# Kernel tuning notes

Measured on AMD Instinct MI355X. Metric: run time of the kernel, lower is better.

The kernel has to match this reference:

```python
import jax, jax.numpy as jnp
import numpy as np

N_NODES = 40000
N_EDGES = 640000
N_GRAPHS = 64
D_IN = 128
D_H = 128
N_LAYERS = 3
EPS = 1e-5


def _layer_norm(x, g, b):
    mu = jnp.mean(x, axis=-1, keepdims=True)
    var = jnp.var(x, axis=-1, keepdims=True)
    return (x - mu) * jax.lax.rsqrt(var + EPS) * g + b


def _sage_conv(x, src, dst, Wl, bl, Wr):
    # mean aggregation of neighbor messages: i <- mean_{j: (j->i)} x_j
    msg = x[src]                                              # [E, d]
    agg = jax.ops.segment_sum(msg, dst, num_segments=N_NODES)  # [N, d]
    deg = jax.ops.segment_sum(jnp.ones((src.shape[0],), x.dtype), dst,
                              num_segments=N_NODES)
    agg = agg / jnp.clip(deg, 1.0)[:, None]
    # out = lin_l(agg) + lin_r(x)
    return agg @ Wl.T + bl + x @ Wr.T


def setup_inputs() -> dict:
    key = jax.random.key(0)
    ks = jax.random.split(key, 12)
    s = 0.05
    x = jax.random.normal(ks[0], (N_NODES, D_IN), jnp.float32)
    edge_index = jax.random.randint(ks[1], (2, N_EDGES), 0, N_NODES, jnp.int64)
    batch = jnp.sort(jax.random.randint(ks[2], (N_NODES,), 0, N_GRAPHS, jnp.int64))
    fc_w = jax.random.normal(ks[3], (D_H, D_IN), jnp.float32) * s
    fc_b = jax.random.normal(ks[4], (D_H,), jnp.float32) * s
    Wl = jax.random.normal(ks[5], (N_LAYERS, D_H, D_H), jnp.float32) * s
    bl = jax.random.normal(ks[6], (N_LAYERS, D_H), jnp.float32) * s
    Wr = jax.random.normal(ks[7], (N_LAYERS, D_H, D_H), jnp.float32) * s
    ln_g = jnp.ones((N_LAYERS - 1, D_H), jnp.float32)
    ln_b = jnp.zeros((N_LAYERS - 1, D_H), jnp.float32)
    return {"x": x, "edge_index": edge_index, "batch": batch,
            "fc_w": fc_w, "fc_b": fc_b, "Wl": Wl, "bl": bl, "Wr": Wr,
            "ln_g": ln_g, "ln_b": ln_b}


def reference(x, edge_index, batch, fc_w, fc_b, Wl, bl, Wr, ln_g, ln_b):
    src, dst = edge_index[0], edge_index[1]
    # input projection + ReLU
    h = jax.nn.relu(x @ fc_w.T + fc_b)
    # GraphSAGE stack: norm + ReLU between layers, none after the last
    for i in range(N_LAYERS):
        h = _sage_conv(h, src, dst, Wl[i], bl[i], Wr[i])
        if i < N_LAYERS - 1:
            h = jax.nn.relu(_layer_norm(h, ln_g[i], ln_b[i]))
    node_embed = h                                            # [N, D_H]
    graph_embed = jax.ops.segment_sum(node_embed, batch,
                                      num_segments=N_GRAPHS)  # [G, D_H]
    return node_embed, graph_embed
```

## Files before the change

kernel.cpp:

```cpp
#include <hip/hip_runtime.h>
#include <hip/hip_bf16.h>


#define N_NODES 40000
#define N_EDGES 640000
#define N_GRAPHS 64
#define D 128
#define NODE_ELEMS 5120000
#define N_TILES 1250
#define ELL_W 64

typedef __hip_bfloat16 bf16;
typedef __attribute__((ext_vector_type(8))) short bf16x8;
typedef __attribute__((ext_vector_type(4))) float f32x4;

__device__ __forceinline__ float b2f(bf16 v) { return __bfloat162float(v); }
__device__ __forceinline__ bf16 f2b(float v) { return __float2bfloat16(v); }
__device__ __forceinline__ float lo2f(unsigned w) { return __uint_as_float(w << 16); }
__device__ __forceinline__ float hi2f(unsigned w) { return __uint_as_float(w & 0xffff0000u); }
__device__ __forceinline__ unsigned packbf(float a, float b) {
    union { bf16 h[2]; unsigned u; } c;
    c.h[0] = f2b(a); c.h[1] = f2b(b);
    return c.u;
}
__device__ __forceinline__ unsigned char f2e4m3(float v) {
    unsigned u = __float_as_uint(v * 0x1p-120f);
    unsigned r = (u + 0x0007ffffu + ((u >> 20) & 1u)) >> 20;
    return (unsigned char)min(r, 0x7eu);
}
__device__ __forceinline__ int is_bf16(const unsigned* lng) {
    return (lng[0] == 0x3f803f80u) ? 1 : 0;
}
__device__ __forceinline__ int edge_is_i64(const void* edge) {
    const unsigned* ew = (const unsigned*)edge;
    return (ew[1] == 0u && ew[3] == 0u && ew[5] == 0u) ? 1 : 0;
}

union U8 { uint4 u; bf16x8 s; };

template <int ISB>
__device__ __forceinline__ bf16x8 load8t(const void* base, long idx) {
    if (ISB) {
        U8 t;
        t.u = *(const uint4*)((const bf16*)base + idx);
        return t.s;
    }
    const float* f = (const float*)base + idx;
    float4 f0 = *(const float4*)f;
    float4 f1 = *(const float4*)(f + 4);
    union { bf16 h[8]; bf16x8 s; } t;
    t.h[0] = f2b(f0.x); t.h[1] = f2b(f0.y); t.h[2] = f2b(f0.z); t.h[3] = f2b(f0.w);
    t.h[4] = f2b(f1.x); t.h[5] = f2b(f1.y); t.h[6] = f2b(f1.z); t.h[7] = f2b(f1.w);
    return t.s;
}

template <int ISB>
__device__ __forceinline__ void proj_body(
    const void* __restrict__ X, const void* __restrict__ fcw,
    const void* __restrict__ fcb, bf16* __restrict__ outb,
    unsigned char* __restrict__ out8, int id, int t,
    bf16 (*sb)[128], unsigned char (*s8)[128]) {
    const int lane = t & 63;
    const int wave = t >> 6;
    const int n = lane & 15, q = lane >> 4;
    const int rowgrp = wave >> 1;
    const int cb = (wave & 1) * 64;
    const f32x4 zero = {0.f, 0.f, 0.f, 0.f};

    bf16x8 wf[4][4];
#pragma unroll
    for (int ct = 0; ct < 4; ct++)
#pragma unroll
        for (int ks = 0; ks < 4; ks++)
            wf[ct][ks] = load8t<ISB>(fcw, (long)(cb + ct * 16 + n) * 128 + ks * 32 + q * 8);
    float bz[4];
#pragma unroll
    for (int ct = 0; ct < 4; ct++)
        bz[ct] = ISB ? b2f(((const bf16*)fcb)[cb + ct * 16 + n])
                     : ((const float*)fcb)[cb + ct * 16 + n];

    for (int tile = id; tile < N_TILES; tile += 512) {
        const long rbase = (long)tile * 32 + rowgrp * 16 + n;
        f32x4 acc[4] = {zero, zero, zero, zero};
        bf16x8 af[4];
#pragma unroll
        for (int ks = 0; ks < 4; ks++)
            af[ks] = load8t<ISB>(X, rbase * 128 + ks * 32 + q * 8);
#pragma unroll
        for (int ct = 0; ct < 4; ct++)
#pragma unroll
            for (int ks = 0; ks < 4; ks++)
                acc[ct] = __builtin_amdgcn_mfma_f32_16x16x32_bf16(
                    af[ks], wf[ct][ks], acc[ct], 0, 0, 0);
#pragma unroll
        for (int ct = 0; ct < 4; ct++) {
            const int col = cb + ct * 16 + n;
#pragma unroll
            for (int r = 0; r < 4; r++) {
                const int rl = rowgrp * 16 + q * 4 + r;
                float v = fmaxf(acc[ct][r] + bz[ct], 0.f);
                sb[rl][col] = f2b(v);
                s8[rl][col] = f2e4m3(v);
            }
        }
        __syncthreads();
        {
            uint4* ob = (uint4*)((char*)outb + (size_t)tile * 8192);
            ob[t] = ((const uint4*)sb)[t];
            ob[t + 256] = ((const uint4*)sb)[t + 256];
            ((uint4*)(out8 + (size_t)tile * 4096))[t] = ((const uint4*)s8)[t];
        }
        __syncthreads();
    }
}

#define CW2_TOTAL 99200
__global__ __launch_bounds__(256, 2) void k_main(
    const void* __restrict__ X, const void* __restrict__ fcw,
    const void* __restrict__ fcb, bf16* __restrict__ outb,
    unsigned char* __restrict__ out8,
    const void* __restrict__ edge, const void* __restrict__ batch,
    const void* Wl, const void* bl, const void* Wr,
    const void* lng, const void* lnb,
    int* __restrict__ cursor, unsigned short* __restrict__ ell,
    int* __restrict__ batch32, bf16* __restrict__ cw,
    float* __restrict__ gsum) {
    __shared__ bf16 sb[32][128];
    __shared__ unsigned char s8[32][128];
    const int bid = blockIdx.x, t = threadIdx.x;
    int role, id;
    if (bid < 1000) { role = (bid & 1) ? 0 : 1; id = bid >> 1; }
    else if (bid < 1012) { role = 0; id = 500 + (bid - 1000); }
    else if (bid < 1169) { role = 2; id = bid - 1012; }
    else { role = 3; id = bid - 1169; }

    if (role == 1) {
        const int i64 = edge_is_i64(edge);
        int s[5], d[5];
#pragma unroll
        for (int i = 0; i < 5; i++) {
            int e = id * 1280 + i * 256 + t;
            if (i64) {
                s[i] = (int)((const long long*)edge)[e];
                d[i] = (int)((const long long*)edge)[N_EDGES + e];
            } else {
                s[i] = ((const int*)edge)[e];
                d[i] = ((const int*)edge)[N_EDGES + e];
            }
        }
        int p[5];
#pragma unroll
        for (int i = 0; i < 5; i++) p[i] = atomicAdd(&cursor[d[i]], 1);
#pragma unroll
        for (int i = 0; i < 5; i++)
            if (p[i] < ELL_W) ell[d[i] * ELL_W + p[i]] = (unsigned short)s[i];
        return;
    }
    if (role == 2) {
        int j = id * 256 + t;
        if (j < N_NODES)
            batch32[j] = edge_is_i64(edge) ? (int)((const long long*)batch)[j]
                                           : ((const int*)batch)[j];
        return;
    }
    if (role == 3) {
        int i = id * 256 + t;
        if (i >= CW2_TOTAL) return;
        int isb = is_bf16((const unsigned*)lng);
        const void* s; int o;
        if (i < 49152)       { s = Wl;  o = i; }
        else if (i < 49536)  { s = bl;  o = i - 49152; }
        else if (i < 98688)  { s = Wr;  o = i - 49536; }
        else if (i < 98944)  { s = lng; o = i - 98688; }
        else                 { s = lnb; o = i - 98944; }
        cw[i] = isb ? ((const bf16*)s)[o] : f2b(((const float*)s)[o]);
        return;
    }

    {
        int i = id * 256 + t;
        if (i < N_GRAPHS * D) gsum[i] = 0.f;
    }
    if (is_bf16((const unsigned*)lng))
        proj_body<1>(X, fcw, fcb, outb, out8, id, t, sb, s8);
    else
        proj_body<0>(X, fcw, fcb, outb, out8, id, t, sb, s8);
}

__global__ __launch_bounds__(256, 6) void k_agg8(
    const unsigned char* __restrict__ h8, const int* __restrict__ cursor,
    const unsigned short* __restrict__ ell, bf16* __restrict__ agg) {
    const int qw = threadIdx.x >> 4;
    const int l16 = threadIdx.x & 15;
    const int nodeA = blockIdx.x * 32 + qw * 2;
    const int nodeB = nodeA + 1;
    const int degA = min(cursor[nodeA], ELL_W);
    const int degB = min(cursor[nodeB], ELL_W);
    const int dmax = max(degA, degB);
    const uint4* rA = (const uint4*)(ell + (size_t)nodeA * ELL_W);
    const uint4* rB = (const uint4*)(ell + (size_t)nodeB * ELL_W);
    const uint2* hp = (const uint2*)h8;
    float aA[8] = {0.f, 0.f, 0.f, 0.f, 0.f, 0.f, 0.f, 0.f};
    float aB[8] = {0.f, 0.f, 0.f, 0.f, 0.f, 0.f, 0.f, 0.f};
    for (int e = 0; e < dmax; e += 8) {
        const uint4 ia = rA[e >> 3];
        const uint4 ib = rB[e >> 3];
        uint2 gA[8], gB[8];
        gA[0] = hp[(size_t)(ia.x & 0xffffu) * 16 + l16];
        gA[1] = hp[(size_t)(ia.x >> 16) * 16 + l16];
        gA[2] = hp[(size_t)(ia.y & 0xffffu) * 16 + l16];
        gA[3] = hp[(size_t)(ia.y >> 16) * 16 + l16];
        gA[4] = hp[(size_t)(ia.z & 0xffffu) * 16 + l16];
        gA[5] = hp[(size_t)(ia.z >> 16) * 16 + l16];
        gA[6] = hp[(size_t)(ia.w & 0xffffu) * 16 + l16];
        gA[7] = hp[(size_t)(ia.w >> 16) * 16 + l16];
        gB[0] = hp[(size_t)(ib.x & 0xffffu) * 16 + l16];
        gB[1] = hp[(size_t)(ib.x >> 16) * 16 + l16];
        gB[2] = hp[(size_t)(ib.y & 0xffffu) * 16 + l16];
        gB[3] = hp[(size_t)(ib.y >> 16) * 16 + l16];
        gB[4] = hp[(size_t)(ib.z & 0xffffu) * 16 + l16];
        gB[5] = hp[(size_t)(ib.z >> 16) * 16 + l16];
        gB[6] = hp[(size_t)(ib.w & 0xffffu) * 16 + l16];
        gB[7] = hp[(size_t)(ib.w >> 16) * 16 + l16];
#pragma unroll
        for (int i = 0; i < 8; i++) {
            const float mA = (e + i < degA) ? 0x1p120f : 0.f;
            aA[0] = fmaf(mA, __uint_as_float((gA[i].x << 20) & 0x07f00000u), aA[0]);
            aA[1] = fmaf(mA, __uint_as_float((gA[i].x << 12) & 0x07f00000u), aA[1]);
            aA[2] = fmaf(mA, __uint_as_float((gA[i].x << 4)  & 0x07f00000u), aA[2]);
            aA[3] = fmaf(mA, __uint_as_float((gA[i].x >> 4)  & 0x07f00000u), aA[3]);
            aA[4] = fmaf(mA, __uint_as_float((gA[i].y << 20) & 0x07f00000u), aA[4]);
            aA[5] = fmaf(mA, __uint_as_float((gA[i].y << 12) & 0x07f00000u), aA[5]);
            aA[6] = fmaf(mA, __uint_as_float((gA[i].y << 4)  & 0x07f00000u), aA[6]);
            aA[7] = fmaf(mA, __uint_as_float((gA[i].y >> 4)  & 0x07f00000u), aA[7]);
        }
#pragma unroll
        for (int i = 0; i < 8; i++) {
            const float mB = (e + i < degB) ? 0x1p120f : 0.f;
            aB[0] = fmaf(mB, __uint_as_float((gB[i].x << 20) & 0x07f00000u), aB[0]);
            aB[1] = fmaf(mB, __uint_as_float((gB[i].x << 12) & 0x07f00000u), aB[1]);
            aB[2] = fmaf(mB, __uint_as_float((gB[i].x << 4)  & 0x07f00000u), aB[2]);
            aB[3] = fmaf(mB, __uint_as_float((gB[i].x >> 4)  & 0x07f00000u), aB[3]);
            aB[4] = fmaf(mB, __uint_as_float((gB[i].y << 20) & 0x07f00000u), aB[4]);
            aB[5] = fmaf(mB, __uint_as_float((gB[i].y << 12) & 0x07f00000u), aB[5]);
            aB[6] = fmaf(mB, __uint_as_float((gB[i].y << 4)  & 0x07f00000u), aB[6]);
            aB[7] = fmaf(mB, __uint_as_float((gB[i].y >> 4)  & 0x07f00000u), aB[7]);
        }
    }
    const float invA = 1.f / (float)max(degA, 1);
    const float invB = 1.f / (float)max(degB, 1);
    uint4 oA, oB;
    oA.x = packbf(aA[0] * invA, aA[1] * invA);
    oA.y = packbf(aA[2] * invA, aA[3] * invA);
    oA.z = packbf(aA[4] * invA, aA[5] * invA);
    oA.w = packbf(aA[6] * invA, aA[7] * invA);
    oB.x = packbf(aB[0] * invB, aB[1] * invB);
    oB.y = packbf(aB[2] * invB, aB[3] * invB);
    oB.z = packbf(aB[4] * invB, aB[5] * invB);
    oB.w = packbf(aB[6] * invB, aB[7] * invB);
    ((uint4*)agg)[(size_t)nodeA * 16 + l16] = oA;
    ((uint4*)agg)[(size_t)nodeB * 16 + l16] = oB;
}

template <int MODE>
__global__ __launch_bounds__(256, 2) void k_gemm(
    const bf16* __restrict__ A, const bf16* __restrict__ W1,
    const bf16* __restrict__ B, const bf16* __restrict__ W2,
    const bf16* __restrict__ bias, bf16* __restrict__ outb,
    unsigned char* __restrict__ out8, void* __restrict__ outx,
    const bf16* __restrict__ lgam, const bf16* __restrict__ lbet,
    const unsigned* __restrict__ lngraw) {
    __shared__ float sred[2][2][16][2];
    __shared__ bf16 sb[32][128];
    __shared__ unsigned char s8[32][128];
    __shared__ float sf[32][128];
    const int tid = threadIdx.x;
    const int lane = tid & 63;
    const int wave = tid >> 6;
    const int n = lane & 15, q = lane >> 4;
    const int rowgrp = wave >> 1;
    const int cbi = wave & 1;
    const int cb = cbi * 64;
    const int isb = is_bf16(lngraw);

    bf16x8 wf[2][4][4];
#pragma unroll
    for (int p = 0; p < 2; p++) {
        const bf16* Wp = p ? W2 : W1;
#pragma unroll
        for (int ct = 0; ct < 4; ct++)
#pragma unroll
            for (int ks = 0; ks < 4; ks++) {
                U8 t;
                t.u = *(const uint4*)&Wp[(cb + ct * 16 + n) * 128 + ks * 32 + q * 8];
                wf[p][ct][ks] = t.s;
            }
    }
    float bz[4], gf[4], bf_[4];
#pragma unroll
    for (int ct = 0; ct < 4; ct++) {
        bz[ct] = b2f(bias[cb + ct * 16 + n]);
        if (MODE == 1) {
            gf[ct] = b2f(lgam[cb + ct * 16 + n]);
            bf_[ct] = b2f(lbet[cb + ct * 16 + n]);
        }
    }

    const f32x4 zero = {0.f, 0.f, 0.f, 0.f};

    for (int tile = blockIdx.x; tile < N_TILES; tile += gridDim.x) {
        const long rbase = (long)tile * 32 + rowgrp * 16 + n;
        f32x4 acc[4] = {zero, zero, zero, zero};
#pragma unroll
        for (int p = 0; p < 2; p++) {
            const bf16* Ap = p ? B : A;
            bf16x8 af[4];
#pragma unroll
            for (int ks = 0; ks < 4; ks++) {
                U8 t;
                t.u = *(const uint4*)&Ap[rbase * 128 + ks * 32 + q * 8];
                af[ks] = t.s;
            }
#pragma unroll
            for (int ct = 0; ct < 4; ct++)
#pragma unroll
                for (int ks = 0; ks < 4; ks++)
                    acc[ct] = __builtin_amdgcn_mfma_f32_16x16x32_bf16(
                        af[ks], wf[p][ct][ks], acc[ct], 0, 0, 0);
        }

        float vs[4][4];
#pragma unroll
        for (int ct = 0; ct < 4; ct++)
#pragma unroll
            for (int r = 0; r < 4; r++) vs[ct][r] = acc[ct][r] + bz[ct];

        if (MODE == 1) {
            float s[4], ss[4];
#pragma unroll
            for (int r = 0; r < 4; r++) {
                s[r] = 0.f; ss[r] = 0.f;
#pragma unroll
                for (int ct = 0; ct < 4; ct++) {
                    s[r] += vs[ct][r];
                    ss[r] += vs[ct][r] * vs[ct][r];
                }
            }
#pragma unroll
            for (int m = 1; m <= 8; m <<= 1)
#pragma unroll
                for (int r = 0; r < 4; r++) {
                    s[r] += __shfl_xor(s[r], m, 64);
                    ss[r] += __shfl_xor(ss[r], m, 64);
                }
            if (n == 0) {
#pragma unroll
                for (int r = 0; r < 4; r++) {
                    sred[rowgrp][cbi][q * 4 + r][0] = s[r];
                    sred[rowgrp][cbi][q * 4 + r][1] = ss[r];
                }
            }
            __syncthreads();
#pragma unroll
            for (int r = 0; r < 4; r++) {
                float S = s[r] + sred[rowgrp][1 - cbi][q * 4 + r][0];
                float SS = ss[r] + sred[rowgrp][1 - cbi][q * 4 + r][1];
                float mu = S * (1.f / 128.f);
                float var = SS * (1.f / 128.f) - mu * mu;
                float rstd = rsqrtf(var + 1e-5f);
#pragma unroll
                for (int ct = 0; ct < 4; ct++)
                    vs[ct][r] = fmaxf((vs[ct][r] - mu) * rstd * gf[ct] + bf_[ct], 0.f);
            }
        }

#pragma unroll
        for (int ct = 0; ct < 4; ct++) {
            const int col = cb + ct * 16 + n;
#pragma unroll
            for (int r = 0; r < 4; r++) {
                const int rl = rowgrp * 16 + q * 4 + r;
                float v = vs[ct][r];
                if (MODE == 1) {
                    sb[rl][col] = f2b(v);
                    s8[rl][col] = f2e4m3(v);
                } else {
                    if (isb) sb[rl][col] = f2b(v);
                    else sf[rl][col] = v;
                }
            }
        }
        __syncthreads();
        if (MODE == 1) {
            uint4* ob = (uint4*)((char*)outb + (size_t)tile * 8192);
            ob[tid] = ((const uint4*)sb)[tid];
            ob[tid + 256] = ((const uint4*)sb)[tid + 256];
            ((uint4*)(out8 + (size_t)tile * 4096))[tid] = ((const uint4*)s8)[tid];
        } else {
            if (isb) {
                uint4* ob = (uint4*)((char*)outx + (size_t)tile * 8192);
                ob[tid] = ((const uint4*)sb)[tid];
                ob[tid + 256] = ((const uint4*)sb)[tid + 256];
            } else {
                uint4* of = (uint4*)((char*)outx + (size_t)tile * 16384);
#pragma unroll
                for (int k = 0; k < 4; k++)
                    of[tid + 256 * k] = ((const uint4*)sf)[tid + 256 * k];
            }
        }
        __syncthreads();
    }
}

__device__ __forceinline__ int lbound(const int* a, int n, int key) {
    int lo = 0, hi = n;
    while (lo < hi) {
        int mid = (lo + hi) >> 1;
        if (a[mid] < key) lo = mid + 1; else hi = mid;
    }
    return lo;
}

__global__ void k_graph(const void* __restrict__ node, const int* __restrict__ batch,
                        float* __restrict__ gsum, const unsigned* __restrict__ lngraw) {
    const int g = blockIdx.x >> 4, part = blockIdx.x & 15;
    const int c = threadIdx.x;
    const int isb = is_bf16(lngraw);
    const int lo = lbound(batch, N_NODES, g);
    const int hi = lbound(batch, N_NODES, g + 1);
    const int len = hi - lo;
    const int b0 = lo + (len * part) / 16;
    const int b1 = lo + (len * (part + 1)) / 16;
    float s0 = 0.f, s1 = 0.f;
    int n = b0;
    if (isb) {
        const bf16* nb = (const bf16*)node;
        for (; n + 2 <= b1; n += 2) {
            s0 += b2f(nb[(size_t)(n + 0) * 128 + c]);
            s1 += b2f(nb[(size_t)(n + 1) * 128 + c]);
        }
        for (; n < b1; n++) s0 += b2f(nb[(size_t)n * 128 + c]);
    } else {
        const float* nf = (const float*)node;
        for (; n + 2 <= b1; n += 2) {
            s0 += nf[(size_t)(n + 0) * 128 + c];
            s1 += nf[(size_t)(n + 1) * 128 + c];
        }
        for (; n < b1; n++) s0 += nf[(size_t)n * 128 + c];
    }
    atomicAdd(&gsum[g * 128 + c], s0 + s1);
}

__global__ void k_gout(const float* __restrict__ gsum, void* __restrict__ out,
                       const unsigned* __restrict__ lngraw) {
    int i = blockIdx.x * 256 + threadIdx.x;
    if (i >= N_GRAPHS * D) return;
    if (is_bf16(lngraw)) ((bf16*)out)[NODE_ELEMS + i] = f2b(gsum[i]);
    else ((float*)out)[NODE_ELEMS + i] = gsum[i];
}

extern "C" void kernel_launch(void* const* d_in, const int* in_sizes, int n_in,
                              void* d_out, int out_size, void* d_ws, size_t ws_size,
                              hipStream_t stream) {
    const void* x = d_in[0];
    const void* edge = d_in[1];
    const void* batch = d_in[2];
    const void* fc_w = d_in[3];
    const void* fc_b = d_in[4];
    const void* Wl = d_in[5];
    const void* bl = d_in[6];
    const void* Wr = d_in[7];
    const void* ln_g = d_in[8];
    const void* ln_b = d_in[9];
    const unsigned* lngraw = (const unsigned*)ln_g;

    size_t off = 0;
    char* base = (char*)d_ws;
    auto carve = [&](size_t bytes) -> char* {
        char* p = base + off;
        off = (off + bytes + 255) & ~(size_t)255;
        return p;
    };
    bf16* cw = (bf16*)carve((size_t)CW2_TOTAL * 2);
    bf16* hA = (bf16*)carve((size_t)NODE_ELEMS * 2);
    bf16* hB = (bf16*)carve((size_t)NODE_ELEMS * 2);
    bf16* agg = (bf16*)carve((size_t)NODE_ELEMS * 2);
    unsigned char* h8A = (unsigned char*)carve((size_t)NODE_ELEMS);
    unsigned char* h8B = (unsigned char*)carve((size_t)NODE_ELEMS);
    int* batch32 = (int*)carve((size_t)N_NODES * 4);
    unsigned short* ell = (unsigned short*)carve((size_t)N_NODES * ELL_W * 2);
    int* cursor = (int*)carve((size_t)N_NODES * 4);
    float* gsum = (float*)carve((size_t)N_GRAPHS * D * 4);

    const bf16* cw_Wl = cw;
    const bf16* cw_bl = cw + 49152;
    const bf16* cw_Wr = cw + 49536;
    const bf16* cw_lng = cw + 98688;
    const bf16* cw_lnb = cw + 98944;

    hipMemsetAsync(cursor, 0, (size_t)N_NODES * 4, stream);
    k_main<<<1557, 256, 0, stream>>>(x, fc_w, fc_b, hA, h8A, edge, batch,
                                     Wl, bl, Wr, ln_g, ln_b,
                                     cursor, ell, batch32, cw, gsum);

    bf16* hcur = hA;
    bf16* hnext = hB;
    unsigned char* h8cur = h8A;
    unsigned char* h8next = h8B;
    for (int l = 0; l < 3; l++) {
        const bf16* W1 = cw_Wl + (size_t)l * 16384;
        const bf16* W2 = cw_Wr + (size_t)l * 16384;
        const bf16* bb = cw_bl + (size_t)l * 128;
        k_agg8<<<1250, 256, 0, stream>>>(h8cur, cursor, ell, agg);
        if (l < 2) {
            k_gemm<1><<<512, 256, 0, stream>>>(agg, W1, hcur, W2, bb, hnext,
                                               h8next, nullptr,
                                               cw_lng + (size_t)l * 128,
                                               cw_lnb + (size_t)l * 128, lngraw);
            bf16* t = hcur; hcur = hnext; hnext = t;
            unsigned char* t8 = h8cur; h8cur = h8next; h8next = t8;
        } else {
            k_gemm<2><<<512, 256, 0, stream>>>(agg, W1, hcur, W2, bb, nullptr,
                                               nullptr, d_out, nullptr, nullptr,
                                               lngraw);
        }
    }

    k_graph<<<1024, 128, 0, stream>>>(d_out, batch32, gsum, lngraw);
    k_gout<<<32, 256, 0, stream>>>(gsum, d_out, lngraw);
}
```

Before: 238.8 us.

## Fuse neighbor aggregation into per-layer GEMM kernel via shared-memory tile

Merges the separate FP8 gather-aggregation kernel and the dual GEMM kernel into one per-tile layer kernel. Each 32-node block first computes the root (x·Wr) MFMA product, then gathers neighbor features into a shared-memory aggregate tile and applies Wl, followed by LayerNorm/ReLU and stores. This removes the bf16 agg buffer round trip through global memory and one launch per layer. In exchange, the persistent grid and register-cached weights are dropped, so weights are reloaded per tile, and gather latency now sits alongside MFMA work at a different occupancy.

Result: slower. 262.8 us (+10.0%).

```diff
diff --git a/kernel.cpp b/kernel.cpp
--- a/kernel.cpp
+++ b/kernel.cpp
@@ -16,8 +16,6 @@
 
 __device__ __forceinline__ float b2f(bf16 v) { return __bfloat162float(v); }
 __device__ __forceinline__ bf16 f2b(float v) { return __float2bfloat16(v); }
-__device__ __forceinline__ float lo2f(unsigned w) { return __uint_as_float(w << 16); }
-__device__ __forceinline__ float hi2f(unsigned w) { return __uint_as_float(w & 0xffff0000u); }
 __device__ __forceinline__ unsigned packbf(float a, float b) {
     union { bf16 h[2]; unsigned u; } c;
     c.h[0] = f2b(a); c.h[1] = f2b(b);
@@ -187,93 +185,21 @@
         proj_body<0>(X, fcw, fcb, outb, out8, id, t, sb, s8);
 }
 
-__global__ __launch_bounds__(256, 6) void k_agg8(
-    const unsigned char* __restrict__ h8, const int* __restrict__ cursor,
-    const unsigned short* __restrict__ ell, bf16* __restrict__ agg) {
-    const int qw = threadIdx.x >> 4;
-    const int l16 = threadIdx.x & 15;
-    const int nodeA = blockIdx.x * 32 + qw * 2;
-    const int nodeB = nodeA + 1;
-    const int degA = min(cursor[nodeA], ELL_W);
-    const int degB = min(cursor[nodeB], ELL_W);
-    const int dmax = max(degA, degB);
-    const uint4* rA = (const uint4*)(ell + (size_t)nodeA * ELL_W);
-    const uint4* rB = (const uint4*)(ell + (size_t)nodeB * ELL_W);
-    const uint2* hp = (const uint2*)h8;
-    float aA[8] = {0.f, 0.f, 0.f, 0.f, 0.f, 0.f, 0.f, 0.f};
-    float aB[8] = {0.f, 0.f, 0.f, 0.f, 0.f, 0.f, 0.f, 0.f};
-    for (int e = 0; e < dmax; e += 8) {
-        const uint4 ia = rA[e >> 3];
-        const uint4 ib = rB[e >> 3];
-        uint2 gA[8], gB[8];
-        gA[0] = hp[(size_t)(ia.x & 0xffffu) * 16 + l16];
-        gA[1] = hp[(size_t)(ia.x >> 16) * 16 + l16];
-        gA[2] = hp[(size_t)(ia.y & 0xffffu) * 16 + l16];
-        gA[3] = hp[(size_t)(ia.y >> 16) * 16 + l16];
-        gA[4] = hp[(size_t)(ia.z & 0xffffu) * 16 + l16];
-        gA[5] = hp[(size_t)(ia.z >> 16) * 16 + l16];
-        gA[6] = hp[(size_t)(ia.w & 0xffffu) * 16 + l16];
-        gA[7] = hp[(size_t)(ia.w >> 16) * 16 + l16];
-        gB[0] = hp[(size_t)(ib.x & 0xffffu) * 16 + l16];
-        gB[1] = hp[(size_t)(ib.x >> 16) * 16 + l16];
-        gB[2] = hp[(size_t)(ib.y & 0xffffu) * 16 + l16];
-        gB[3] = hp[(size_t)(ib.y >> 16) * 16 + l16];
-        gB[4] = hp[(size_t)(ib.z & 0xffffu) * 16 + l16];
-        gB[5] = hp[(size_t)(ib.z >> 16) * 16 + l16];
-        gB[6] = hp[(size_t)(ib.w & 0xffffu) * 16 + l16];
-        gB[7] = hp[(size_t)(ib.w >> 16) * 16 + l16];
-#pragma unroll
-        for (int i = 0; i < 8; i++) {
-            const float mA = (e + i < degA) ? 0x1p120f : 0.f;
-            aA[0] = fmaf(mA, __uint_as_float((gA[i].x << 20) & 0x07f00000u), aA[0]);
-            aA[1] = fmaf(mA, __uint_as_float((gA[i].x << 12) & 0x07f00000u), aA[1]);
-            aA[2] = fmaf(mA, __uint_as_float((gA[i].x << 4)  & 0x07f00000u), aA[2]);
-            aA[3] = fmaf(mA, __uint_as_float((gA[i].x >> 4)  & 0x07f00000u), aA[3]);
-            aA[4] = fmaf(mA, __uint_as_float((gA[i].y << 20) & 0x07f00000u), aA[4]);
-            aA[5] = fmaf(mA, __uint_as_float((gA[i].y << 12) & 0x07f00000u), aA[5]);
-            aA[6] = fmaf(mA, __uint_as_float((gA[i].y << 4)  & 0x07f00000u), aA[6]);
-            aA[7] = fmaf(mA, __uint_as_float((gA[i].y >> 4)  & 0x07f00000u), aA[7]);
-        }
-#pragma unroll
-        for (int i = 0; i < 8; i++) {
-            const float mB = (e + i < degB) ? 0x1p120f : 0.f;
-            aB[0] = fmaf(mB, __uint_as_float((gB[i].x << 20) & 0x07f00000u), aB[0]);
-            aB[1] = fmaf(mB, __uint_as_float((gB[i].x << 12) & 0x07f00000u), aB[1]);
-            aB[2] = fmaf(mB, __uint_as_float((gB[i].x << 4)  & 0x07f00000u), aB[2]);
-            aB[3] = fmaf(mB, __uint_as_float((gB[i].x >> 4)  & 0x07f00000u), aB[3]);
-            aB[4] = fmaf(mB, __uint_as_float((gB[i].y << 20) & 0x07f00000u), aB[4]);
-            aB[5] = fmaf(mB, __uint_as_float((gB[i].y << 12) & 0x07f00000u), aB[5]);
-            aB[6] = fmaf(mB, __uint_as_float((gB[i].y << 4)  & 0x07f00000u), aB[6]);
-            aB[7] = fmaf(mB, __uint_as_float((gB[i].y >> 4)  & 0x07f00000u), aB[7]);
-        }
-    }
-    const float invA = 1.f / (float)max(degA, 1);
-    const float invB = 1.f / (float)max(degB, 1);
-    uint4 oA, oB;
-    oA.x = packbf(aA[0] * invA, aA[1] * invA);
-    oA.y = packbf(aA[2] * invA, aA[3] * invA);
-    oA.z = packbf(aA[4] * invA, aA[5] * invA);
-    oA.w = packbf(aA[6] * invA, aA[7] * invA);
-    oB.x = packbf(aB[0] * invB, aB[1] * invB);
-    oB.y = packbf(aB[2] * invB, aB[3] * invB);
-    oB.z = packbf(aB[4] * invB, aB[5] * invB);
-    oB.w = packbf(aB[6] * invB, aB[7] * invB);
-    ((uint4*)agg)[(size_t)nodeA * 16 + l16] = oA;
-    ((uint4*)agg)[(size_t)nodeB * 16 + l16] = oB;
-}
-
 template <int MODE>
-__global__ __launch_bounds__(256, 2) void k_gemm(
-    const bf16* __restrict__ A, const bf16* __restrict__ W1,
-    const bf16* __restrict__ B, const bf16* __restrict__ W2,
+__global__ __launch_bounds__(256, 4) void k_layer(
+    const bf16* __restrict__ h, const unsigned char* __restrict__ h8,
+    const int* __restrict__ cursor, const unsigned short* __restrict__ ell,
+    const bf16* __restrict__ W1, const bf16* __restrict__ W2,
     const bf16* __restrict__ bias, bf16* __restrict__ outb,
     unsigned char* __restrict__ out8, void* __restrict__ outx,
     const bf16* __restrict__ lgam, const bf16* __restrict__ lbet,
     const unsigned* __restrict__ lngraw) {
+    __shared__ bf16 sagg[32][136];
     __shared__ float sred[2][2][16][2];
     __shared__ bf16 sb[32][128];
     __shared__ unsigned char s8[32][128];
     __shared__ float sf[32][128];
+    const int tile = blockIdx.x;
     const int tid = threadIdx.x;
     const int lane = tid & 63;
     const int wave = tid >> 6;
@@ -282,133 +208,205 @@
     const int cbi = wave & 1;
     const int cb = cbi * 64;
     const int isb = is_bf16(lngraw);
-
-    bf16x8 wf[2][4][4];
-#pragma unroll
-    for (int p = 0; p < 2; p++) {
-        const bf16* Wp = p ? W2 : W1;
+    const f32x4 zero = {0.f, 0.f, 0.f, 0.f};
+
+    const long rbase = (long)tile * 32 + rowgrp * 16 + n;
+    f32x4 acc[4] = {zero, zero, zero, zero};
+    {
+        bf16x8 af[4];
+#pragma unroll
+        for (int ks = 0; ks < 4; ks++) {
+            U8 u;
+            u.u = *(const uint4*)&h[rbase * 128 + ks * 32 + q * 8];
+            af[ks] = u.s;
+        }
 #pragma unroll
         for (int ct = 0; ct < 4; ct++)
 #pragma unroll
             for (int ks = 0; ks < 4; ks++) {
-                U8 t;
-                t.u = *(const uint4*)&Wp[(cb + ct * 16 + n) * 128 + ks * 32 + q * 8];
-                wf[p][ct][ks] = t.s;
-            }
-    }
-    float bz[4], gf[4], bf_[4];
+                U8 w;
+                w.u = *(const uint4*)&W2[(cb + ct * 16 + n) * 128 + ks * 32 + q * 8];
+                acc[ct] = __builtin_amdgcn_mfma_f32_16x16x32_bf16(
+                    af[ks], w.s, acc[ct], 0, 0, 0);
+            }
+    }
+
+    {
+        const int qw = tid >> 4;
+        const int l16 = tid & 15;
+        const int nodeA = tile * 32 + qw * 2;
+        const int nodeB = nodeA + 1;
+        const int degA = min(cursor[nodeA], ELL_W);
+        const int degB = min(cursor[nodeB], ELL_W);
+        const int dmax = max(degA, degB);
+        const uint4* rA = (const uint4*)(ell + (size_t)nodeA * ELL_W);
+        const uint4* rB = (const uint4*)(ell + (size_t)nodeB * ELL_W);
+        const uint2* hp = (const uint2*)h8;
+        float aA[8] = {0.f, 0.f, 0.f, 0.f, 0.f, 0.f, 0.f, 0.f};
+        float aB[8] = {0.f, 0.f, 0.f, 0.f, 0.f, 0.f, 0.f, 0.f};
+        for (int e = 0; e < dmax; e += 8) {
+            const uint4 ia = rA[e >> 3];
+            const uint4 ib = rB[e >> 3];
+            uint2 gA[8], gB[8];
+            gA[0] = hp[(size_t)(ia.x & 0xffffu) * 16 + l16];
+            gA[1] = hp[(size_t)(ia.x >> 16) * 16 + l16];
+            gA[2] = hp[(size_t)(ia.y & 0xffffu) * 16 + l16];
+            gA[3] = hp[(size_t)(ia.y >> 16) * 16 + l16];
+            gA[4] = hp[(size_t)(ia.z & 0xffffu) * 16 + l16];
+            gA[5] = hp[(size_t)(ia.z >> 16) * 16 + l16];
+            gA[6] = hp[(size_t)(ia.w & 0xffffu) * 16 + l16];
+            gA[7] = hp[(size_t)(ia.w >> 16) * 16 + l16];
+            gB[0] = hp[(size_t)(ib.x & 0xffffu) * 16 + l16];
+            gB[1] = hp[(size_t)(ib.x >> 16) * 16 + l16];
+            gB[2] = hp[(size_t)(ib.y & 0xffffu) * 16 + l16];
+            gB[3] = hp[(size_t)(ib.y >> 16) * 16 + l16];
+            gB[4] = hp[(size_t)(ib.z & 0xffffu) * 16 + l16];
+            gB[5] = hp[(size_t)(ib.z >> 16) * 16 + l16];
+            gB[6] = hp[(size_t)(ib.w & 0xffffu) * 16 + l16];
+            gB[7] = hp[(size_t)(ib.w >> 16) * 16 + l16];
+#pragma unroll
+            for (int i = 0; i < 8; i++) {
+                const float mA = (e + i < degA) ? 0x1p120f : 0.f;
+                aA[0] = fmaf(mA, __uint_as_float((gA[i].x << 20) & 0x07f00000u), aA[0]);
+                aA[1] = fmaf(mA, __uint_as_float((gA[i].x << 12) & 0x07f00000u), aA[1]);
+                aA[2] = fmaf(mA, __uint_as_float((gA[i].x << 4)  & 0x07f00000u), aA[2]);
+                aA[3] = fmaf(mA, __uint_as_float((gA[i].x >> 4)  & 0x07f00000u), aA[3]);
+                aA[4] = fmaf(mA, __uint_as_float((gA[i].y << 20) & 0x07f00000u), aA[4]);
+                aA[5] = fmaf(mA, __uint_as_float((gA[i].y << 12) & 0x07f00000u), aA[5]);
+                aA[6] = fmaf(mA, __uint_as_float((gA[i].y << 4)  & 0x07f00000u), aA[6]);
+                aA[7] = fmaf(mA, __uint_as_float((gA[i].y >> 4)  & 0x07f00000u), aA[7]);
+            }
+#pragma unroll
+            for (int i = 0; i < 8; i++) {
+                const float mB = (e + i < degB) ? 0x1p120f : 0.f;
+                aB[0] = fmaf(mB, __uint_as_float((gB[i].x << 20) & 0x07f00000u), aB[0]);
+                aB[1] = fmaf(mB, __uint_as_float((gB[i].x << 12) & 0x07f00000u), aB[1]);
+                aB[2] = fmaf(mB, __uint_as_float((gB[i].x << 4)  & 0x07f00000u), aB[2]);
+                aB[3] = fmaf(mB, __uint_as_float((gB[i].x >> 4)  & 0x07f00000u), aB[3]);
+                aB[4] = fmaf(mB, __uint_as_float((gB[i].y << 20) & 0x07f00000u), aB[4]);
+                aB[5] = fmaf(mB, __uint_as_float((gB[i].y << 12) & 0x07f00000u), aB[5]);
+                aB[6] = fmaf(mB, __uint_as_float((gB[i].y << 4)  & 0x07f00000u), aB[6]);
+                aB[7] = fmaf(mB, __uint_as_float((gB[i].y >> 4)  & 0x07f00000u), aB[7]);
+            }
+        }
+        const float invA = 1.f / (float)max(degA, 1);
+        const float invB = 1.f / (float)max(degB, 1);
+        uint4 oA, oB;
+        oA.x = packbf(aA[0] * invA, aA[1] * invA);
+        oA.y = packbf(aA[2] * invA, aA[3] * invA);
+        oA.z = packbf(aA[4] * invA, aA[5] * invA);
+        oA.w = packbf(aA[6] * invA, aA[7] * invA);
+        oB.x = packbf(aB[0] * invB, aB[1] * invB);
+        oB.y = packbf(aB[2] * invB, aB[3] * invB);
+        oB.z = packbf(aB[4] * invB, aB[5] * invB);
+        oB.w = packbf(aB[6] * invB, aB[7] * invB);
+        *(uint4*)&sagg[qw * 2][l16 * 8] = oA;
+        *(uint4*)&sagg[qw * 2 + 1][l16 * 8] = oB;
+    }
+    __syncthreads();
+
+    {
+        bf16x8 ag[4];
+#pragma unroll
+        for (int ks = 0; ks < 4; ks++)
+            ag[ks] = *(const bf16x8*)&sagg[rowgrp * 16 + n][ks * 32 + q * 8];
+#pragma unroll
+        for (int ct = 0; ct < 4; ct++)
+#pragma unroll
+            for (int ks = 0; ks < 4; ks++) {
+                U8 w;
+                w.u = *(const uint4*)&W1[(cb + ct * 16 + n) * 128 + ks * 32 + q * 8];
+                acc[ct] = __builtin_amdgcn_mfma_f32_16x16x32_bf16(
+                    ag[ks], w.s, acc[ct], 0, 0, 0);
+            }
+    }
+
+    float vs[4][4];
 #pragma unroll
     for (int ct = 0; ct < 4; ct++) {
-        bz[ct] = b2f(bias[cb + ct * 16 + n]);
-        if (MODE == 1) {
+        const float bz = b2f(bias[cb + ct * 16 + n]);
+#pragma unroll
+        for (int r = 0; r < 4; r++) vs[ct][r] = acc[ct][r] + bz;
+    }
+
+    if (MODE == 1) {
+        float gf[4], bf_[4];
+#pragma unroll
+        for (int ct = 0; ct < 4; ct++) {
             gf[ct] = b2f(lgam[cb + ct * 16 + n]);
             bf_[ct] = b2f(lbet[cb + ct * 16 + n]);
         }
-    }
-
-    const f32x4 zero = {0.f, 0.f, 0.f, 0.f};
-
-    for (int tile = blockIdx.x; tile < N_TILES; tile += gridDim.x) {
-        const long rbase = (long)tile * 32 + rowgrp * 16 + n;
-        f32x4 acc[4] = {zero, zero, zero, zero};
-#pragma unroll
-        for (int p = 0; p < 2; p++) {
-            const bf16* Ap = p ? B : A;
-            bf16x8 af[4];
-#pragma unroll
-            for (int ks = 0; ks < 4; ks++) {
-                U8 t;
-                t.u = *(const uint4*)&Ap[rbase * 128 + ks * 32 + q * 8];
-                af[ks] = t.s;
-            }
+        float s[4], ss[4];
+#pragma unroll
+        for (int r = 0; r < 4; r++) {
+            s[r] = 0.f; ss[r] = 0.f;
+#pragma unroll
+            for (int ct = 0; ct < 4; ct++) {
+                s[r] += vs[ct][r];
+                ss[r] += vs[ct][r] * vs[ct][r];
+            }
+        }
+#pragma unroll
+        for (int m = 1; m <= 8; m <<= 1)
+#pragma unroll
+            for (int r = 0; r < 4; r++) {
+                s[r] += __shfl_xor(s[r], m, 64);
+                ss[r] += __shfl_xor(ss[r], m, 64);
+            }
+        if (n == 0) {
+#pragma unroll
+            for (int r = 0; r < 4; r++) {
+                sred[rowgrp][cbi][q * 4 + r][0] = s[r];
+                sred[rowgrp][cbi][q * 4 + r][1] = ss[r];
+            }
+        }
+        __syncthreads();
+#pragma unroll
+        for (int r = 0; r < 4; r++) {
+            float S = s[r] + sred[rowgrp][1 - cbi][q * 4 + r][0];
+            float SS = ss[r] + sred[rowgrp][1 - cbi][q * 4 + r][1];
+            float mu = S * (1.f / 128.f);
+            float var = SS * (1.f / 128.f) - mu * mu;
+            float rstd = rsqrtf(var + 1e-5f);
 #pragma unroll
             for (int ct = 0; ct < 4; ct++)
-#pragma unroll
-                for (int ks = 0; ks < 4; ks++)
-                    acc[ct] = __builtin_amdgcn_mfma_f32_16x16x32_bf16(
-                        af[ks], wf[p][ct][ks], acc[ct], 0, 0, 0);
-        }
-
-        float vs[4][4];
-#pragma unroll
-        for (int ct = 0; ct < 4; ct++)
-#pragma unroll
-            for (int r = 0; r < 4; r++) vs[ct][r] = acc[ct][r] + bz[ct];
-
-        if (MODE == 1) {
-            float s[4], ss[4];
-#pragma unroll
-            for (int r = 0; r < 4; r++) {
-                s[r] = 0.f; ss[r] = 0.f;
-#pragma unroll
-                for (int ct = 0; ct < 4; ct++) {
-                    s[r] += vs[ct][r];
-                    ss[r] += vs[ct][r] * vs[ct][r];
-                }
-            }
-#pragma unroll
-            for (int m = 1; m <= 8; m <<= 1)
-#pragma unroll
-                for (int r = 0; r < 4; r++) {
-                    s[r] += __shfl_xor(s[r], m, 64);
-                    ss[r] += __shfl_xor(ss[r], m, 64);
-                }
-            if (n == 0) {
-#pragma unroll
-                for (int r = 0; r < 4; r++) {
-                    sred[rowgrp][cbi][q * 4 + r][0] = s[r];
-                    sred[rowgrp][cbi][q * 4 + r][1] = ss[r];
-                }
-            }
-            __syncthreads();
-#pragma unroll
-            for (int r = 0; r < 4; r++) {
-                float S = s[r] + sred[rowgrp][1 - cbi][q * 4 + r][0];
-                float SS = ss[r] + sred[rowgrp][1 - cbi][q * 4 + r][1];
-                float mu = S * (1.f / 128.f);
-                float var = SS * (1.f / 128.f) - mu * mu;
-                float rstd = rsqrtf(var + 1e-5f);
-#pragma unroll
-                for (int ct = 0; ct < 4; ct++)
-                    vs[ct][r] = fmaxf((vs[ct][r] - mu) * rstd * gf[ct] + bf_[ct], 0.f);
-            }
-        }
-
-#pragma unroll
-        for (int ct = 0; ct < 4; ct++) {
-            const int col = cb + ct * 16 + n;
-#pragma unroll
-            for (int r = 0; r < 4; r++) {
-                const int rl = rowgrp * 16 + q * 4 + r;
-                float v = vs[ct][r];
-                if (MODE == 1) {
-                    sb[rl][col] = f2b(v);
-                    s8[rl][col] = f2e4m3(v);
-                } else {
-                    if (isb) sb[rl][col] = f2b(v);
-                    else sf[rl][col] = v;
-                }
-            }
-        }
-        __syncthreads();
-        if (MODE == 1) {
-            uint4* ob = (uint4*)((char*)outb + (size_t)tile * 8192);
+                vs[ct][r] = fmaxf((vs[ct][r] - mu) * rstd * gf[ct] + bf_[ct], 0.f);
+        }
+    }
+
+#pragma unroll
+    for (int ct = 0; ct < 4; ct++) {
+        const int col = cb + ct * 16 + n;
+#pragma unroll
+        for (int r = 0; r < 4; r++) {
+            const int rl = rowgrp * 16 + q * 4 + r;
+            float v = vs[ct][r];
+            if (MODE == 1) {
+                sb[rl][col] = f2b(v);
+                s8[rl][col] = f2e4m3(v);
+            } else {
+                if (isb) sb[rl][col] = f2b(v);
+                else sf[rl][col] = v;
+            }
+        }
+    }
+    __syncthreads();
+    if (MODE == 1) {
+        uint4* ob = (uint4*)((char*)outb + (size_t)tile * 8192);
+        ob[tid] = ((const uint4*)sb)[tid];
+        ob[tid + 256] = ((const uint4*)sb)[tid + 256];
+        ((uint4*)(out8 + (size_t)tile * 4096))[tid] = ((const uint4*)s8)[tid];
+    } else {
+        if (isb) {
+            uint4* ob = (uint4*)((char*)outx + (size_t)tile * 8192);
             ob[tid] = ((const uint4*)sb)[tid];
             ob[tid + 256] = ((const uint4*)sb)[tid + 256];
-            ((uint4*)(out8 + (size_t)tile * 4096))[tid] = ((const uint4*)s8)[tid];
         } else {
-            if (isb) {
-                uint4* ob = (uint4*)((char*)outx + (size_t)tile * 8192);
-                ob[tid] = ((const uint4*)sb)[tid];
-                ob[tid + 256] = ((const uint4*)sb)[tid + 256];
-            } else {
-                uint4* of = (uint4*)((char*)outx + (size_t)tile * 16384);
-#pragma unroll
-                for (int k = 0; k < 4; k++)
-                    of[tid + 256 * k] = ((const uint4*)sf)[tid + 256 * k];
-            }
-        }
-        __syncthreads();
+            uint4* of = (uint4*)((char*)outx + (size_t)tile * 16384);
+#pragma unroll
+            for (int k = 0; k < 4; k++)
+                of[tid + 256 * k] = ((const uint4*)sf)[tid + 256 * k];
+        }
     }
 }
 
@@ -484,7 +482,6 @@
     bf16* cw = (bf16*)carve((size_t)CW2_TOTAL * 2);
     bf16* hA = (bf16*)carve((size_t)NODE_ELEMS * 2);
     bf16* hB = (bf16*)carve((size_t)NODE_ELEMS * 2);
-    bf16* agg = (bf16*)carve((size_t)NODE_ELEMS * 2);
     unsigned char* h8A = (unsigned char*)carve((size_t)NODE_ELEMS);
     unsigned char* h8B = (unsigned char*)carve((size_t)NODE_ELEMS);
     int* batch32 = (int*)carve((size_t)N_NODES * 4);
@@ -511,18 +508,16 @@
         const bf16* W1 = cw_Wl + (size_t)l * 16384;
         const bf16* W2 = cw_Wr + (size_t)l * 16384;
         const bf16* bb = cw_bl + (size_t)l * 128;
-        k_agg8<<<1250, 256, 0, stream>>>(h8cur, cursor, ell, agg);
         if (l < 2) {
-            k_gemm<1><<<512, 256, 0, stream>>>(agg, W1, hcur, W2, bb, hnext,
-                                               h8next, nullptr,
-                                               cw_lng + (size_t)l * 128,
-                                               cw_lnb + (size_t)l * 128, lngraw);
+            k_layer<1><<<N_TILES, 256, 0, stream>>>(
+                hcur, h8cur, cursor, ell, W1, W2, bb, hnext, h8next, nullptr,
+                cw_lng + (size_t)l * 128, cw_lnb + (size_t)l * 128, lngraw);
             bf16* t = hcur; hcur = hnext; hnext = t;
             unsigned char* t8 = h8cur; h8cur = h8next; h8next = t8;
         } else {
-            k_gemm<2><<<512, 256, 0, stream>>>(agg, W1, hcur, W2, bb, nullptr,
-                                               nullptr, d_out, nullptr, nullptr,
-                                               lngraw);
+            k_layer<2><<<N_TILES, 256, 0, stream>>>(
+                hcur, h8cur, cursor, ell, W1, W2, bb, nullptr, nullptr, d_out,
+                nullptr, nullptr, lngraw);
         }
     }
 
```
